# Optimization experiments

Hardware: AMD Instinct MI355X
Metric: run time of the kernel (lower is better)

## Reference

```python
import jax, jax.numpy as jnp
import numpy as np

T = 2048          # num tokens (single long prefill sequence)
HID = 2048        # hidden_size
NH = 16           # num query heads
NKV = 2           # num kv heads
HD = 128          # head_dim (kv_channels)
ROPE_BASE = 10000.0


def setup_inputs() -> dict:
    key = jax.random.key(0)
    k1, k2, k3, k4, k5 = jax.random.split(key, 5)
    s = 0.02
    return {
        "hidden_states": jax.random.normal(k1, (T, HID), dtype=jnp.float32),
        "positions": jnp.arange(T, dtype=jnp.int64 if jax.config.jax_enable_x64 else jnp.int32),
        "Wq": jax.random.normal(k2, (NH * HD, HID), dtype=jnp.float32) * s,
        "Wk": jax.random.normal(k3, (NKV * HD, HID), dtype=jnp.float32) * s,
        "Wv": jax.random.normal(k4, (NKV * HD, HID), dtype=jnp.float32) * s,
        "Wo": jax.random.normal(k5, (HID, NH * HD), dtype=jnp.float32) * s,
    }


def _rope_cos_sin(positions):
    # fp32 RoPE tables, HF-style (concat of freqs with itself)
    inv_freq = 1.0 / (ROPE_BASE ** (jnp.arange(0, HD, 2, dtype=jnp.float32) / HD))
    freqs = positions.astype(jnp.float32)[:, None] * inv_freq[None, :]   # [T, HD/2]
    emb = jnp.concatenate([freqs, freqs], axis=-1)                        # [T, HD]
    return jnp.cos(emb)[:, None, :], jnp.sin(emb)[:, None, :]             # [T,1,HD]


def _rotate_half(x):
    x1, x2 = jnp.split(x, 2, axis=-1)
    return jnp.concatenate([-x2, x1], axis=-1)


def reference(hidden_states, positions, Wq, Wk, Wv, Wo):
    dtype = hidden_states.dtype
    # fused QKV projection (weights concatenated once, single GEMM)
    W_fused = jnp.concatenate([Wq, Wk, Wv], axis=0)            # [q+2kv, HID]
    qkv = hidden_states @ W_fused.T                             # [T, q+2kv]
    q, k, v = jnp.split(qkv, [NH * HD, NH * HD + NKV * HD], axis=-1)

    # fp32 RoPE on q/k
    cos, sin = _rope_cos_sin(positions)                         # [T,1,HD]
    qf = q.reshape(T, NH, HD).astype(jnp.float32)
    kf = k.reshape(T, NKV, HD).astype(jnp.float32)
    qf = qf * cos + _rotate_half(qf) * sin
    kf = kf * cos + _rotate_half(kf) * sin
    q = qf.astype(dtype)                                        # [T,NH,HD]
    k = kf.astype(dtype)                                        # [T,NKV,HD]
    v = v.reshape(T, NKV, HD)

    # causal GQA attention (same math as the paged-attention kernel on one seq)
    group = NH // NKV
    k_rep = jnp.repeat(k, group, axis=1)                        # [T,NH,HD]
    v_rep = jnp.repeat(v, group, axis=1)                        # [T,NH,HD]
    scale = HD ** -0.5
    scores = jnp.einsum('qhd,khd->hqk', q, k_rep) * scale       # [NH,T,T]
    causal = jnp.tril(jnp.ones((T, T), dtype=bool))
    scores = jnp.where(causal[None], scores, jnp.finfo(scores.dtype).min)
    probs = jax.nn.softmax(scores, axis=-1)
    attn = jnp.einsum('hqk,khd->qhd', probs, v_rep).reshape(T, NH * HD)

    return attn @ Wo.T                                          # [T, HID]
```

## Files before the change

kernel.cpp:

```cpp
#include <hip/hip_runtime.h>

#define T_TOK 2048
#define HID   2048
#define NH    16
#define NKV   2
#define HD    128
#define QDIM  (NH * HD)
#define KVDIM (NKV * HD)
#define QKVDIM (QDIM + 2 * KVDIM)

typedef float          f32x4  __attribute__((ext_vector_type(4)));
typedef unsigned short u16x8  __attribute__((ext_vector_type(8)));
typedef __bf16         bf16x8 __attribute__((ext_vector_type(8)));

__device__ __forceinline__ unsigned short f2bf(float f) {
    __bf16 h = (__bf16)f;
    return __builtin_bit_cast(unsigned short, h);
}

__device__ __forceinline__ f32x4 mfma16(u16x8 a, u16x8 b, f32x4 c) {
    return __builtin_amdgcn_mfma_f32_16x16x32_bf16(
        __builtin_bit_cast(bf16x8, a), __builtin_bit_cast(bf16x8, b), c, 0, 0, 0);
}

#define QSCL 0.12751743f
#define DEFER_THR 11.5416f

__global__ __launch_bounds__(256) void pack_bf16_all(
    const float* __restrict__ hidden, const float* __restrict__ Wq,
    const float* __restrict__ Wk, const float* __restrict__ Wv,
    const float* __restrict__ Wo, const int* __restrict__ positions,
    unsigned short* __restrict__ hb, unsigned short* __restrict__ Wf,
    unsigned short* __restrict__ Wob, float* __restrict__ ctab)
{
    const int b = blockIdx.x;
    if (b >= 6656) {
        const int bb = b - 6656;
        const int t  = bb * 4 + (threadIdx.x >> 6);
        const int j  = threadIdx.x & 63;
        float invf = expf(-(float)j * 0.14391156831212787f);
        float f = (float)positions[t] * invf;
        ctab[(size_t)t * 128 + j]      = cosf(f);
        ctab[(size_t)t * 128 + 64 + j] = sinf(f);
        return;
    }
    const float* src; unsigned short* dst; size_t off;
    if      (b < 2048) { src = hidden; dst = hb;            off = (size_t)b * 2048; }
    else if (b < 4096) { src = Wq;     dst = Wf;            off = (size_t)(b - 2048) * 2048; }
    else if (b < 4352) { src = Wk;     dst = Wf + 4194304;  off = (size_t)(b - 4096) * 2048; }
    else if (b < 4608) { src = Wv;     dst = Wf + 4718592;  off = (size_t)(b - 4352) * 2048; }
    else               { src = Wo;     dst = Wob;           off = (size_t)(b - 4608) * 2048; }

    const size_t i = off + threadIdx.x * 8;
    float4 f0 = *reinterpret_cast<const float4*>(src + i);
    float4 f1 = *reinterpret_cast<const float4*>(src + i + 4);
    u16x8 o;
    o[0]=f2bf(f0.x); o[1]=f2bf(f0.y); o[2]=f2bf(f0.z); o[3]=f2bf(f0.w);
    o[4]=f2bf(f1.x); o[5]=f2bf(f1.y); o[6]=f2bf(f1.z); o[7]=f2bf(f1.w);
    *reinterpret_cast<u16x8*>(dst + i) = o;
}

__global__ __launch_bounds__(256) void qkv_gemm_fused(
    const unsigned short* __restrict__ A,
    const unsigned short* __restrict__ B,
    const float* __restrict__ ctab,
    unsigned short* __restrict__ qr,
    unsigned short* __restrict__ kr,
    unsigned short* __restrict__ vt)
{
    __shared__ alignas(16) char smem[49152];
    unsigned short* AsBase = (unsigned short*)smem;
    unsigned short* BsBase = (unsigned short*)(smem + 16384);

    const int tid  = threadIdx.x;
    const int lane = tid & 63;
    const int w    = tid >> 6;
    const int lg   = lane >> 4, lc = lane & 15;

    const int nbx = QKVDIM / 128;
    const int cpx = gridDim.x >> 3;
    const int wg  = (blockIdx.x & 7) * cpx + (blockIdx.x >> 3);
    const int m0  = (wg / nbx) * 64, n0 = (wg % nbx) * 128;

    const int rowL = lane >> 3;
    const int gS   = (lane & 7) ^ rowL;
    const int wr   = (w >> 1) * 32, wc = (w & 1) * 64;

    f32x4 acc[2][4] = {};

    auto stage = [&](int buf, int kb) {
        #pragma unroll
        for (int ci = 0; ci < 2; ci++) {
            const int chunk = w * 2 + ci;
            const int row   = chunk * 8 + rowL;
            const unsigned short* gpA = &A[(size_t)(m0 + row) * HID + kb + gS * 8];
            __builtin_amdgcn_global_load_lds(
                (const __attribute__((address_space(1))) void*)gpA,
                (__attribute__((address_space(3))) void*)(&AsBase[buf * 4096 + chunk * 512]),
                16, 0, 0);
        }
        #pragma unroll
        for (int ci = 0; ci < 4; ci++) {
            const int chunk = w * 4 + ci;
            const int row   = chunk * 8 + rowL;
            const unsigned short* gpB = &B[(size_t)(n0 + row) * HID + kb + gS * 8];
            __builtin_amdgcn_global_load_lds(
                (const __attribute__((address_space(1))) void*)gpB,
                (__attribute__((address_space(3))) void*)(&BsBase[buf * 8192 + chunk * 512]),
                16, 0, 0);
        }
    };

    stage(0, 0);
    const int nk = HID >> 6;
    for (int t = 0; t < nk; ++t) {
        if (t + 1 < nk) {
            stage((t + 1) & 1, (t + 1) * 64);
            asm volatile("s_waitcnt vmcnt(6)" ::: "memory");
        } else {
            asm volatile("s_waitcnt vmcnt(0)" ::: "memory");
        }
        __syncthreads();

        const unsigned short* As_ = &AsBase[(t & 1) * 4096];
        const unsigned short* Bs_ = &BsBase[(t & 1) * 8192];
        #pragma unroll
        for (int kk = 0; kk < 2; kk++) {
            u16x8 af[2], bf[4];
            const int g = (kk * 4 + lg) ^ (lc & 7);
            #pragma unroll
            for (int mi = 0; mi < 2; mi++) {
                const int r = wr + mi * 16 + lc;
                af[mi] = *reinterpret_cast<const u16x8*>(&As_[r * 64 + g * 8]);
            }
            #pragma unroll
            for (int ni = 0; ni < 4; ni++) {
                const int r = wc + ni * 16 + lc;
                bf[ni] = *reinterpret_cast<const u16x8*>(&Bs_[r * 64 + g * 8]);
            }
            #pragma unroll
            for (int mi = 0; mi < 2; mi++)
                #pragma unroll
                for (int ni = 0; ni < 4; ni++)
                    acc[mi][ni] = mfma16(af[mi], bf[ni], acc[mi][ni]);
        }
        __syncthreads();
    }

    if (n0 < QDIM + KVDIM) {
        float* Ep = (float*)smem;
        #pragma unroll
        for (int mi = 0; mi < 2; mi++)
            #pragma unroll
            for (int ni = 0; ni < 4; ni++)
                #pragma unroll
                for (int j = 0; j < 4; j++)
                    Ep[(wr + mi * 16 + lg * 4 + j) * 132 + wc + ni * 16 + lc]
                        = acc[mi][ni][j];
        __syncthreads();

        const bool isq = (n0 < QDIM);
        const float scl = isq ? QSCL : 1.0f;
        unsigned short* dst  = isq ? qr : kr;
        const int rowstride  = isq ? QDIM : KVDIM;
        const int colbase    = isq ? n0 : (n0 - QDIM);

        const int r  = tid >> 2;
        const int jb = (tid & 3) * 16;
        const float* ct = ctab + (size_t)(m0 + r) * 128;
        unsigned short* drow = dst + (size_t)(m0 + r) * rowstride + colbase;
        #pragma unroll
        for (int g = 0; g < 4; g++) {
            ushort4 p1, p2;
            #pragma unroll
            for (int e = 0; e < 4; e++) {
                const int j = jb + g * 4 + e;
                float x1 = Ep[r * 132 + j];
                float x2 = Ep[r * 132 + j + 64];
                float c = ct[j], s = ct[64 + j];
                ((unsigned short*)&p1)[e] = f2bf((x1 * c - x2 * s) * scl);
                ((unsigned short*)&p2)[e] = f2bf((x2 * c + x1 * s) * scl);
            }
            *reinterpret_cast<ushort4*>(drow + jb + g * 4)      = p1;
            *reinterpret_cast<ushort4*>(drow + jb + g * 4 + 64) = p2;
        }
    } else {
        #pragma unroll
        for (int mi = 0; mi < 2; mi++)
            #pragma unroll
            for (int ni = 0; ni < 4; ni++) {
                const int d   = (n0 - QDIM - KVDIM) + wc + ni * 16 + lc;
                const int t0r = m0 + wr + mi * 16 + lg * 4;
                ushort4 pk;
                pk.x = f2bf(acc[mi][ni][0]);
                pk.y = f2bf(acc[mi][ni][1]);
                pk.z = f2bf(acc[mi][ni][2]);
                pk.w = f2bf(acc[mi][ni][3]);
                *reinterpret_cast<ushort4*>(&vt[(size_t)d * T_TOK + t0r]) = pk;
            }
    }
}

__global__ __launch_bounds__(256) void gemm_out(
    const unsigned short* __restrict__ A,
    const unsigned short* __restrict__ B,
    float* __restrict__ C)
{
    __shared__ alignas(16) unsigned short As[2][64 * 64];
    __shared__ alignas(16) unsigned short Bs[2][128 * 64];

    const int tid  = threadIdx.x;
    const int lane = tid & 63;
    const int w    = tid >> 6;
    const int lg   = lane >> 4, lc = lane & 15;

    const int nbx = HID / 128;
    const int cpx = gridDim.x >> 3;
    const int wg  = (blockIdx.x & 7) * cpx + (blockIdx.x >> 3);
    const int m0  = (wg / nbx) * 64, n0 = (wg % nbx) * 128;

    const int rowL = lane >> 3;
    const int gS   = (lane & 7) ^ rowL;
    const int wr   = (w >> 1) * 32, wc = (w & 1) * 64;

    f32x4 acc[2][4] = {};

    auto stage = [&](int buf, int kb) {
        #pragma unroll
        for (int ci = 0; ci < 2; ci++) {
            const int chunk = w * 2 + ci;
            const int row   = chunk * 8 + rowL;
            const unsigned short* gpA = &A[(size_t)(m0 + row) * QDIM + kb + gS * 8];
            __builtin_amdgcn_global_load_lds(
                (const __attribute__((address_space(1))) void*)gpA,
                (__attribute__((address_space(3))) void*)(&As[buf][chunk * 512]),
                16, 0, 0);
        }
        #pragma unroll
        for (int ci = 0; ci < 4; ci++) {
            const int chunk = w * 4 + ci;
            const int row   = chunk * 8 + rowL;
            const unsigned short* gpB = &B[(size_t)(n0 + row) * QDIM + kb + gS * 8];
            __builtin_amdgcn_global_load_lds(
                (const __attribute__((address_space(1))) void*)gpB,
                (__attribute__((address_space(3))) void*)(&Bs[buf][chunk * 512]),
                16, 0, 0);
        }
    };

    stage(0, 0);
    const int nk = QDIM >> 6;
    for (int t = 0; t < nk; ++t) {
        if (t + 1 < nk) {
            stage((t + 1) & 1, (t + 1) * 64);
            asm volatile("s_waitcnt vmcnt(6)" ::: "memory");
        } else {
            asm volatile("s_waitcnt vmcnt(0)" ::: "memory");
        }
        __syncthreads();

        const unsigned short* As_ = As[t & 1];
        const unsigned short* Bs_ = Bs[t & 1];
        #pragma unroll
        for (int kk = 0; kk < 2; kk++) {
            u16x8 af[2], bf[4];
            const int g = (kk * 4 + lg) ^ (lc & 7);
            #pragma unroll
            for (int mi = 0; mi < 2; mi++) {
                const int r = wr + mi * 16 + lc;
                af[mi] = *reinterpret_cast<const u16x8*>(&As_[r * 64 + g * 8]);
            }
            #pragma unroll
            for (int ni = 0; ni < 4; ni++) {
                const int r = wc + ni * 16 + lc;
                bf[ni] = *reinterpret_cast<const u16x8*>(&Bs_[r * 64 + g * 8]);
            }
            #pragma unroll
            for (int mi = 0; mi < 2; mi++)
                #pragma unroll
                for (int ni = 0; ni < 4; ni++)
                    acc[mi][ni] = mfma16(af[mi], bf[ni], acc[mi][ni]);
        }
        __syncthreads();
    }

    #pragma unroll
    for (int mi = 0; mi < 2; mi++)
        #pragma unroll
        for (int ni = 0; ni < 4; ni++)
            #pragma unroll
            for (int j = 0; j < 4; j++)
                C[(size_t)(m0 + wr + mi * 16 + lg * 4 + j) * HID
                  + n0 + wc + ni * 16 + lc] = acc[mi][ni][j];
}

__global__ __launch_bounds__(256) void attn_kernel(
    const unsigned short* __restrict__ q,
    const unsigned short* __restrict__ k,
    const unsigned short* __restrict__ vt,
    unsigned short* __restrict__ o,
    float* __restrict__ pO,
    float* __restrict__ pML)
{
    __shared__ alignas(16) unsigned short Ks[64 * 128];
    __shared__ alignas(16) unsigned short Vs[128 * 64];
    __shared__ alignas(16) unsigned short P[4][16][72];

    const int tid  = threadIdx.x;
    const int lane = tid & 63;
    const int w    = tid >> 6;
    const int lg   = lane >> 4, lc = lane & 15;
    const int b    = blockIdx.x;
    const int h    = b & 15;
    const int idx  = b >> 4;

    int tau, c0;
    if (idx <= 16)      { tau = 15 + idx; c0 = 0; }
    else if (idx == 17) { tau = 31;       c0 = 1; }
    else {
        int j = idx - 18, kk = 15 - (j >> 1);
        if ((j & 1) == 0) { tau = kk - 1;  c0 = 0; }
        else              { tau = kk + 15; c0 = 1; }
    }
    const int kstart = c0 << 4;
    const int kcnt   = min(16, tau + 1 - kstart);

    const int q0   = tau * 64 + w * 16;
    const int hk   = h >> 3;
    const int xr   = (lc & 7) << 4;

    const int krow_l = (lane >> 4);
    const int kgS    = (lane & 15);
    const int vrow_l = (lane >> 3);
    const int vgS    = (lane & 7);

    u16x8 qf[4];
    #pragma unroll
    for (int dc = 0; dc < 4; dc++)
        qf[dc] = *reinterpret_cast<const u16x8*>(
            &q[(size_t)(q0 + lc) * QDIM + h * HD + dc * 32 + lg * 8]);

    float mrow = -1e30f, ell = 0.f;
    f32x4 oacc[8] = {};

    auto stage = [&](int kb) {
        #pragma unroll
        for (int ci = 0; ci < 4; ci++) {
            const int chunk = w * 4 + ci;
            const int row   = chunk * 4 + krow_l;
            const int gSk   = kgS ^ (row & 7);
            const unsigned short* gp =
                &k[(size_t)(kb + row) * KVDIM + hk * HD + gSk * 8];
            __builtin_amdgcn_global_load_lds(
                (const __attribute__((address_space(1))) void*)gp,
                (__attribute__((address_space(3))) void*)(&Ks[chunk * 512]),
                16, 0, 0);
        }
        #pragma unroll
        for (int ci = 0; ci < 4; ci++) {
            const int chunk = w * 4 + ci;
            const int dr    = chunk * 8 + vrow_l;
            const int gSv   = vgS ^ (dr & 7);
            const unsigned short* gp =
                &vt[(size_t)(hk * HD + dr) * T_TOK + kb + gSv * 8];
            __builtin_amdgcn_global_load_lds(
                (const __attribute__((address_space(1))) void*)gp,
                (__attribute__((address_space(3))) void*)(&Vs[chunk * 512]),
                16, 0, 0);
        }
    };

    for (int it = 0; it < kcnt; ++it) {
        const int kb = (kstart + it) * 64;
        stage(kb);
        asm volatile("s_waitcnt vmcnt(4)" ::: "memory");
        __syncthreads();

        const char* KsB = (const char*)Ks;
        const char* VsB = (const char*)Vs;

        float sc[4][4];
        const bool dia = (kb + 63 > q0);
        #pragma unroll
        for (int c4 = 0; c4 < 4; c4++) {
            const int row = c4 * 16 + lc;
            f32x4 s = {0.f, 0.f, 0.f, 0.f};
            #pragma unroll
            for (int dc = 0; dc < 4; dc++) {
                u16x8 kf = *reinterpret_cast<const u16x8*>(
                    KsB + row * 256 + ((dc * 64 + lg * 16) ^ xr));
                s = mfma16(kf, qf[dc], s);
            }
            if (dia) {
                #pragma unroll
                for (int j = 0; j < 4; j++) {
                    const int kpos = kb + c4 * 16 + lg * 4 + j;
                    sc[c4][j] = (kpos <= q0 + lc) ? s[j] : -1e30f;
                }
            } else {
                #pragma unroll
                for (int j = 0; j < 4; j++) sc[c4][j] = s[j];
            }
        }

        float t01 = fmaxf(fmaxf(sc[0][0], sc[0][1]), fmaxf(sc[0][2], sc[0][3]));
        float t23 = fmaxf(fmaxf(sc[1][0], sc[1][1]), fmaxf(sc[1][2], sc[1][3]));
        float t45 = fmaxf(fmaxf(sc[2][0], sc[2][1]), fmaxf(sc[2][2], sc[2][3]));
        float t67 = fmaxf(fmaxf(sc[3][0], sc[3][1]), fmaxf(sc[3][2], sc[3][3]));
        float tmx = fmaxf(fmaxf(t01, t23), fmaxf(t45, t67));
        tmx = fmaxf(tmx, __shfl_xor(tmx, 16));
        tmx = fmaxf(tmx, __shfl_xor(tmx, 32));

        float mn;
        if (__all(tmx <= mrow + DEFER_THR)) {
            mn = mrow;
        } else {
            mn = fmaxf(mrow, tmx);
            float alpha = __builtin_amdgcn_exp2f(mrow - mn);
            mrow = mn;
            ell *= alpha;
            float aj[4];
            #pragma unroll
            for (int j = 0; j < 4; j++)
                aj[j] = __shfl(alpha, lg * 4 + j);
            #pragma unroll
            for (int d8 = 0; d8 < 8; d8++)
                #pragma unroll
                for (int j = 0; j < 4; j++)
                    oacc[d8][j] *= aj[j];
        }

        float rs = 0.f;
        #pragma unroll
        for (int c4 = 0; c4 < 4; c4++) {
            float p0 = __builtin_amdgcn_exp2f(sc[c4][0] - mn);
            float p1 = __builtin_amdgcn_exp2f(sc[c4][1] - mn);
            float p2 = __builtin_amdgcn_exp2f(sc[c4][2] - mn);
            float p3 = __builtin_amdgcn_exp2f(sc[c4][3] - mn);
            rs += (p0 + p1) + (p2 + p3);
            ushort4 pk;
            pk.x = f2bf(p0); pk.y = f2bf(p1); pk.z = f2bf(p2); pk.w = f2bf(p3);
            *reinterpret_cast<ushort4*>(&P[w][lc][c4 * 16 + lg * 4]) = pk;
        }
        rs += __shfl_xor(rs, 16);
        rs += __shfl_xor(rs, 32);
        ell += rs;

        asm volatile("s_waitcnt vmcnt(0) lgkmcnt(0)" ::: "memory");
        __builtin_amdgcn_sched_barrier(0);
        __syncthreads();

        u16x8 pf0 = *reinterpret_cast<const u16x8*>(&P[w][lc][lg * 8]);
        u16x8 pf1 = *reinterpret_cast<const u16x8*>(&P[w][lc][32 + lg * 8]);

        #pragma unroll
        for (int d8 = 0; d8 < 8; d8++) {
            const int drow = d8 * 16 + lc;
            u16x8 vf0 = *reinterpret_cast<const u16x8*>(
                VsB + drow * 128 + ((lg * 16) ^ xr));
            u16x8 vf1 = *reinterpret_cast<const u16x8*>(
                VsB + drow * 128 + ((lg * 16 + 64) ^ xr));
            oacc[d8] = mfma16(pf0, vf0, oacc[d8]);
            oacc[d8] = mfma16(pf1, vf1, oacc[d8]);
        }
        if (it + 1 < kcnt) __syncthreads();
    }

    if (tau < 16) {
        float ej[4];
        #pragma unroll
        for (int j = 0; j < 4; j++)
            ej[j] = __shfl(ell, lg * 4 + j);
        #pragma unroll
        for (int d8 = 0; d8 < 8; d8++)
            #pragma unroll
            for (int j = 0; j < 4; j++) {
                float val = oacc[d8][j] / ej[j];
                o[(size_t)(q0 + lg * 4 + j) * QDIM + h * HD + d8 * 16 + lc] = f2bf(val);
            }
    } else {
        const int s = (h * 16 + (tau - 16)) * 2 + c0;
        float* po = pO + (size_t)s * 8192;
        #pragma unroll
        for (int d8 = 0; d8 < 8; d8++)
            #pragma unroll
            for (int j = 0; j < 4; j++)
                po[(w * 16 + lg * 4 + j) * 128 + d8 * 16 + lc] = oacc[d8][j];
        if (lg == 0) {
            pML[s * 128 + w * 16 + lc]      = mrow;
            pML[s * 128 + 64 + w * 16 + lc] = ell;
        }
    }
}

__global__ __launch_bounds__(256) void attn_combine(
    const float* __restrict__ pO,
    const float* __restrict__ pML,
    unsigned short* __restrict__ o)
{
    const int b  = blockIdx.x;
    const int h  = b >> 4, ti = b & 15;
    const int tau = 16 + ti;
    const int s0 = (h * 16 + ti) * 2, s1 = s0 + 1;

    const int tid = threadIdx.x;
    const int r   = tid >> 2;
    const int cg  = (tid & 3) * 32;

    const float m1 = pML[s0 * 128 + r],      m2 = pML[s1 * 128 + r];
    const float l1 = pML[s0 * 128 + 64 + r], l2 = pML[s1 * 128 + 64 + r];
    const float M  = fmaxf(m1, m2);
    const float w1 = __builtin_amdgcn_exp2f(m1 - M);
    const float w2 = __builtin_amdgcn_exp2f(m2 - M);
    const float rn = 1.0f / (w1 * l1 + w2 * l2);

    const float* o1 = pO + (size_t)s0 * 8192 + r * 128 + cg;
    const float* o2 = pO + (size_t)s1 * 8192 + r * 128 + cg;
    unsigned short* dst = o + (size_t)(tau * 64 + r) * QDIM + h * HD + cg;

    #pragma unroll
    for (int i = 0; i < 8; i++) {
        float4 a = *reinterpret_cast<const float4*>(o1 + i * 4);
        float4 c = *reinterpret_cast<const float4*>(o2 + i * 4);
        ushort4 pk;
        pk.x = f2bf((w1 * a.x + w2 * c.x) * rn);
        pk.y = f2bf((w1 * a.y + w2 * c.y) * rn);
        pk.z = f2bf((w1 * a.z + w2 * c.z) * rn);
        pk.w = f2bf((w1 * a.w + w2 * c.w) * rn);
        *reinterpret_cast<ushort4*>(dst + i * 4) = pk;
    }
}

extern "C" void kernel_launch(void* const* d_in, const int* in_sizes, int n_in,
                              void* d_out, int out_size, void* d_ws, size_t ws_size,
                              hipStream_t stream) {
    const float* hidden    = (const float*)d_in[0];
    const int*   positions = (const int*)d_in[1];
    const float* Wq        = (const float*)d_in[2];
    const float* Wk        = (const float*)d_in[3];
    const float* Wv        = (const float*)d_in[4];
    const float* Wo        = (const float*)d_in[5];
    float*       out       = (float*)d_out;

    char* ws = (char*)d_ws;
    float* pO   = (float*)(ws);
    float* pML  = (float*)(ws + 16777216);
    float* ctab = (float*)(ws + 17039360);
    unsigned short* qr  = (unsigned short*)(ws + 20971520);
    unsigned short* kr  = (unsigned short*)(ws + 29360128);
    unsigned short* vt  = (unsigned short*)(ws + 30408704);
    unsigned short* att = (unsigned short*)(ws + 31457280);
    unsigned short* hb  = (unsigned short*)(ws + 39845888);
    unsigned short* Wf  = (unsigned short*)(ws + 48234496);
    unsigned short* Wob = (unsigned short*)(ws + 58720256);

    pack_bf16_all<<<7168, 256, 0, stream>>>(hidden, Wq, Wk, Wv, Wo, positions,
                                            hb, Wf, Wob, ctab);
    qkv_gemm_fused<<<640, 256, 0, stream>>>(hb, Wf, ctab, qr, kr, vt);
    attn_kernel<<<NH * 48, 256, 0, stream>>>(qr, kr, vt, att, pO, pML);
    attn_combine<<<256, 256, 0, stream>>>(pO, pML, att);
    gemm_out<<<512, 256, 0, stream>>>(att, Wob, out);
}
```

Before: 127.9 us.

## Rebalance causal attention work with table-driven split-KV schedule and 3-way combine

Replaces the fixed 2-way split of long query tiles with a precomputed table of 63 work items per head. Each item covers at most 11 KV blocks, and longer tiles are split into 2 or 3 chunks, so blocks get more even work and the tail is shorter. The combine kernel now merges 2 or 3 partials per tile. The P scratch tile drops its padding and uses an XOR swizzle to avoid LDS bank conflicts. The workspace layout is reshuffled so partial outputs reuse the hb/Wf regions. This adds more partial-write traffic and a more complex layout in exchange for better load balance.

```diff
diff --git a/kernel.cpp b/kernel.cpp
--- a/kernel.cpp
+++ b/kernel.cpp
@@ -25,6 +25,45 @@
 
 #define QSCL 0.12751743f
 #define DEFER_THR 11.5416f
+
+__device__ __forceinline__ float* slotO(char* b, int s) {
+    return (float*)(s < 576 ? b + 47185920 + (size_t)s * 32768
+                            : b + (size_t)(s - 576) * 32768);
+}
+#define PML_OFF 66060288
+
+__device__ const unsigned char S_TAU[63] = {
+ 10,20,21,21,30,31,31,
+  9,18,19,19,20,27,28,28,29,29,29,30,30,31,
+  8,16,17,17,18,24,25,25,26,26,26,27,27,28,
+  7,14,15,15,16,22,22,23,23,23,24,24,25,
+  6,12,13,13,14,22,
+  5,11,11,12,
+  4,3,2,1,0 };
+__device__ const unsigned char S_CST[63] = {
+  0,0,0,11,0,0,11,
+  0,0,0,10,11,0,0,10,0,10,20,11,21,22,
+  0,0,0,9,10,0,0,9,0,9,18,10,19,20,
+  0,0,0,8,9,0,8,0,8,16,9,17,18,
+  0,0,0,7,8,16,
+  0,0,6,7,
+  0,0,0,0,0 };
+__device__ const unsigned char S_CNT[63] = {
+ 11,11,11,11,11,11,11,
+ 10,10,10,10,10,10,10,10,10,10,10,10,10,10,
+  9,9,9,9,9,9,9,9,9,9,9,9,9,9,
+  8,8,8,8,8,8,8,8,8,8,8,8,8,
+  7,7,7,7,7,7,
+  6,6,6,6,
+  5,4,3,2,1 };
+__device__ const unsigned char S_SLT[63] = {
+ 255,18,20,21,46,49,50,
+ 255,14,16,17,19,37,40,41,43,44,45,47,48,51,
+ 255,10,12,13,15,28,31,32,34,35,36,38,39,42,
+ 255,6,8,9,11,22,23,25,26,27,29,30,33,
+ 255,2,4,5,7,24,
+ 255,0,1,3,
+ 255,255,255,255,255 };
 
 __global__ __launch_bounds__(256) void pack_bf16_all(
     const float* __restrict__ hidden, const float* __restrict__ Wq,
@@ -299,12 +338,11 @@
     const unsigned short* __restrict__ k,
     const unsigned short* __restrict__ vt,
     unsigned short* __restrict__ o,
-    float* __restrict__ pO,
-    float* __restrict__ pML)
+    char* __restrict__ wsb)
 {
     __shared__ alignas(16) unsigned short Ks[64 * 128];
     __shared__ alignas(16) unsigned short Vs[128 * 64];
-    __shared__ alignas(16) unsigned short P[4][16][72];
+    __shared__ alignas(16) unsigned short P[4][16][64];
 
     const int tid  = threadIdx.x;
     const int lane = tid & 63;
@@ -312,18 +350,12 @@
     const int lg   = lane >> 4, lc = lane & 15;
     const int b    = blockIdx.x;
     const int h    = b & 15;
-    const int idx  = b >> 4;
-
-    int tau, c0;
-    if (idx <= 16)      { tau = 15 + idx; c0 = 0; }
-    else if (idx == 17) { tau = 31;       c0 = 1; }
-    else {
-        int j = idx - 18, kk = 15 - (j >> 1);
-        if ((j & 1) == 0) { tau = kk - 1;  c0 = 0; }
-        else              { tau = kk + 15; c0 = 1; }
-    }
-    const int kstart = c0 << 4;
-    const int kcnt   = min(16, tau + 1 - kstart);
+    const int e    = b >> 4;
+
+    const int tau    = S_TAU[e];
+    const int kstart = S_CST[e];
+    const int kcnt   = S_CNT[e];
+    const int slt    = S_SLT[e];
 
     const int q0   = tau * 64 + w * 16;
     const int hk   = h >> 3;
@@ -342,6 +374,8 @@
 
     float mrow = -1e30f, ell = 0.f;
     f32x4 oacc[8] = {};
+
+    char* Pw = (char*)P + w * 2048 + lc * 128;
 
     auto stage = [&](int kb) {
         #pragma unroll
@@ -440,7 +474,7 @@
             rs += (p0 + p1) + (p2 + p3);
             ushort4 pk;
             pk.x = f2bf(p0); pk.y = f2bf(p1); pk.z = f2bf(p2); pk.w = f2bf(p3);
-            *reinterpret_cast<ushort4*>(&P[w][lc][c4 * 16 + lg * 4]) = pk;
+            *reinterpret_cast<ushort4*>(Pw + ((c4 * 32 + lg * 8) ^ xr)) = pk;
         }
         rs += __shfl_xor(rs, 16);
         rs += __shfl_xor(rs, 32);
@@ -450,8 +484,8 @@
         __builtin_amdgcn_sched_barrier(0);
         __syncthreads();
 
-        u16x8 pf0 = *reinterpret_cast<const u16x8*>(&P[w][lc][lg * 8]);
-        u16x8 pf1 = *reinterpret_cast<const u16x8*>(&P[w][lc][32 + lg * 8]);
+        u16x8 pf0 = *reinterpret_cast<const u16x8*>(Pw + ((lg * 16) ^ xr));
+        u16x8 pf1 = *reinterpret_cast<const u16x8*>(Pw + ((64 + lg * 16) ^ xr));
 
         #pragma unroll
         for (int d8 = 0; d8 < 8; d8++) {
@@ -466,7 +500,7 @@
         if (it + 1 < kcnt) __syncthreads();
     }
 
-    if (tau < 16) {
+    if (slt == 255) {
         float ej[4];
         #pragma unroll
         for (int j = 0; j < 4; j++)
@@ -479,55 +513,67 @@
                 o[(size_t)(q0 + lg * 4 + j) * QDIM + h * HD + d8 * 16 + lc] = f2bf(val);
             }
     } else {
-        const int s = (h * 16 + (tau - 16)) * 2 + c0;
-        float* po = pO + (size_t)s * 8192;
+        const int slot = h * 52 + slt;
+        float* po = slotO(wsb, slot);
+        float* pML = (float*)(wsb + PML_OFF);
         #pragma unroll
         for (int d8 = 0; d8 < 8; d8++)
             #pragma unroll
             for (int j = 0; j < 4; j++)
                 po[(w * 16 + lg * 4 + j) * 128 + d8 * 16 + lc] = oacc[d8][j];
         if (lg == 0) {
-            pML[s * 128 + w * 16 + lc]      = mrow;
-            pML[s * 128 + 64 + w * 16 + lc] = ell;
+            pML[slot * 128 + w * 16 + lc]      = mrow;
+            pML[slot * 128 + 64 + w * 16 + lc] = ell;
         }
     }
 }
 
 __global__ __launch_bounds__(256) void attn_combine(
-    const float* __restrict__ pO,
-    const float* __restrict__ pML,
+    char* __restrict__ wsb,
     unsigned short* __restrict__ o)
 {
-    const int b  = blockIdx.x;
-    const int h  = b >> 4, ti = b & 15;
-    const int tau = 16 + ti;
-    const int s0 = (h * 16 + ti) * 2, s1 = s0 + 1;
+    const int tau = 11 + blockIdx.x;
+    const int h   = blockIdx.y;
+    const int nch = (tau <= 21) ? 2 : 3;
+    const int sb  = h * 52 + (tau <= 21 ? (tau - 11) * 2 : 22 + (tau - 22) * 3);
+    const float* pML = (const float*)(wsb + PML_OFF);
 
     const int tid = threadIdx.x;
     const int r   = tid >> 2;
     const int cg  = (tid & 3) * 32;
 
-    const float m1 = pML[s0 * 128 + r],      m2 = pML[s1 * 128 + r];
-    const float l1 = pML[s0 * 128 + 64 + r], l2 = pML[s1 * 128 + 64 + r];
-    const float M  = fmaxf(m1, m2);
-    const float w1 = __builtin_amdgcn_exp2f(m1 - M);
-    const float w2 = __builtin_amdgcn_exp2f(m2 - M);
-    const float rn = 1.0f / (w1 * l1 + w2 * l2);
-
-    const float* o1 = pO + (size_t)s0 * 8192 + r * 128 + cg;
-    const float* o2 = pO + (size_t)s1 * 8192 + r * 128 + cg;
+    float m0v = pML[(sb + 0) * 128 + r], l0v = pML[(sb + 0) * 128 + 64 + r];
+    float m1v = pML[(sb + 1) * 128 + r], l1v = pML[(sb + 1) * 128 + 64 + r];
+    float m2v = -1e30f, l2v = 0.f;
+    if (nch > 2) { m2v = pML[(sb + 2) * 128 + r]; l2v = pML[(sb + 2) * 128 + 64 + r]; }
+
+    const float M  = fmaxf(fmaxf(m0v, m1v), m2v);
+    const float w0 = __builtin_amdgcn_exp2f(m0v - M);
+    const float w1 = __builtin_amdgcn_exp2f(m1v - M);
+    const float w2 = nch > 2 ? __builtin_amdgcn_exp2f(m2v - M) : 0.f;
+    const float rn = 1.0f / (w0 * l0v + w1 * l1v + w2 * l2v);
+
+    const float* o0 = slotO(wsb, sb + 0) + r * 128 + cg;
+    const float* o1 = slotO(wsb, sb + 1) + r * 128 + cg;
+    const float* o2 = slotO(wsb, sb + 2) + r * 128 + cg;
     unsigned short* dst = o + (size_t)(tau * 64 + r) * QDIM + h * HD + cg;
 
     #pragma unroll
-    for (int i = 0; i < 8; i++) {
-        float4 a = *reinterpret_cast<const float4*>(o1 + i * 4);
-        float4 c = *reinterpret_cast<const float4*>(o2 + i * 4);
+    for (int g = 0; g < 8; g++) {
+        float4 a0 = *reinterpret_cast<const float4*>(o0 + g * 4);
+        float4 a1 = *reinterpret_cast<const float4*>(o1 + g * 4);
+        float ax = w0 * a0.x + w1 * a1.x;
+        float ay = w0 * a0.y + w1 * a1.y;
+        float az = w0 * a0.z + w1 * a1.z;
+        float aw = w0 * a0.w + w1 * a1.w;
+        if (nch > 2) {
+            float4 a2 = *reinterpret_cast<const float4*>(o2 + g * 4);
+            ax += w2 * a2.x; ay += w2 * a2.y; az += w2 * a2.z; aw += w2 * a2.w;
+        }
         ushort4 pk;
-        pk.x = f2bf((w1 * a.x + w2 * c.x) * rn);
-        pk.y = f2bf((w1 * a.y + w2 * c.y) * rn);
-        pk.z = f2bf((w1 * a.z + w2 * c.z) * rn);
-        pk.w = f2bf((w1 * a.w + w2 * c.w) * rn);
-        *reinterpret_cast<ushort4*>(dst + i * 4) = pk;
+        pk.x = f2bf(ax * rn); pk.y = f2bf(ay * rn);
+        pk.z = f2bf(az * rn); pk.w = f2bf(aw * rn);
+        *reinterpret_cast<ushort4*>(dst + g * 4) = pk;
     }
 }
 
@@ -543,21 +589,19 @@
     float*       out       = (float*)d_out;
 
     char* ws = (char*)d_ws;
-    float* pO   = (float*)(ws);
-    float* pML  = (float*)(ws + 16777216);
-    float* ctab = (float*)(ws + 17039360);
-    unsigned short* qr  = (unsigned short*)(ws + 20971520);
-    unsigned short* kr  = (unsigned short*)(ws + 29360128);
-    unsigned short* vt  = (unsigned short*)(ws + 30408704);
-    unsigned short* att = (unsigned short*)(ws + 31457280);
-    unsigned short* hb  = (unsigned short*)(ws + 39845888);
-    unsigned short* Wf  = (unsigned short*)(ws + 48234496);
-    unsigned short* Wob = (unsigned short*)(ws + 58720256);
+    unsigned short* hb   = (unsigned short*)(ws);
+    unsigned short* Wf   = (unsigned short*)(ws + 8388608);
+    float*          ctab = (float*)(ws + 18874368);
+    unsigned short* qr   = (unsigned short*)(ws + 19922944);
+    unsigned short* kr   = (unsigned short*)(ws + 28311552);
+    unsigned short* vt   = (unsigned short*)(ws + 29360128);
+    unsigned short* att  = (unsigned short*)(ws + 30408704);
+    unsigned short* Wob  = (unsigned short*)(ws + 38797312);
 
     pack_bf16_all<<<7168, 256, 0, stream>>>(hidden, Wq, Wk, Wv, Wo, positions,
                                             hb, Wf, Wob, ctab);
     qkv_gemm_fused<<<640, 256, 0, stream>>>(hb, Wf, ctab, qr, kr, vt);
-    attn_kernel<<<NH * 48, 256, 0, stream>>>(qr, kr, vt, att, pO, pML);
-    attn_combine<<<256, 256, 0, stream>>>(pO, pML, att);
+    attn_kernel<<<NH * 63, 256, 0, stream>>>(qr, kr, vt, att, ws);
+    attn_combine<<<dim3(21, 16), 256, 0, stream>>>(ws, att);
     gemm_out<<<512, 256, 0, stream>>>(att, Wob, out);
 }
```

After: 142.1 us. 1.11x slower.
